# Kernel tuning notes

Measured on AMD Instinct MI355X. Metric: run time of the kernel, lower is better.

The kernel has to match this reference:

```python
import jax, jax.numpy as jnp
import numpy as np

E = 2048      # enc_size
B = 64        # number of output buffer slices (leaves)
STEPS = 2 * B - 1  # 63 reduces then 64 shifts


def _res(x, W, b):
    # ResLayer: residual + ReLU MLP, x: (E,)
    return x + jax.nn.relu(x @ W + b)


def setup_inputs() -> dict:
    key = jax.random.key(0)
    ks = jax.random.split(key, 12)
    s = 1.0 / np.sqrt(E)
    inp = {
        "input_encoding": jax.random.normal(ks[0], (E,), dtype=jnp.float32),
        # 63 ones (reduce) followed by 64 zeros (shift): valid shift-reduce tree
        "fixed_actions": jnp.concatenate([jnp.ones((B - 1,), jnp.int64 if jax.config.jax_enable_x64 else jnp.int32),
                                          jnp.zeros((B,), jnp.int64 if jax.config.jax_enable_x64 else jnp.int32)]),
        # act_scorer: ResLayer + Linear(E, 2)
        "act_res_W": jax.random.normal(ks[1], (E, E), jnp.float32) * s,
        "act_res_b": jnp.zeros((E,), jnp.float32),
        "act_W": jax.random.normal(ks[2], (E, 2), jnp.float32) * s,
        "act_b": jnp.zeros((2,), jnp.float32),
        # unreduce_l: two ResLayers
        "ul1_W": jax.random.normal(ks[3], (E, E), jnp.float32) * s,
        "ul1_b": jnp.zeros((E,), jnp.float32),
        "ul2_W": jax.random.normal(ks[4], (E, E), jnp.float32) * s,
        "ul2_b": jnp.zeros((E,), jnp.float32),
        # unreduce_r: two ResLayers
        "ur1_W": jax.random.normal(ks[5], (E, E), jnp.float32) * s,
        "ur1_b": jnp.zeros((E,), jnp.float32),
        "ur2_W": jax.random.normal(ks[6], (E, E), jnp.float32) * s,
        "ur2_b": jnp.zeros((E,), jnp.float32),
    }
    return inp


def reference(input_encoding, act_res_W, act_res_b, act_W, act_b,
              ul1_W, ul1_b, ul2_W, ul2_b, ur1_W, ur1_b, ur2_W, ur2_b,
              fixed_actions):
    # fixed_actions is a constant action sequence -> Python-level unroll of the
    # data-dependent stack machine (faithful to the torch while-loop).
    acts = np.asarray(fixed_actions)
    stack = [input_encoding]
    buffer_slices = []
    logit_rec = []
    for step in range(acts.shape[0]):
        a = int(acts[step])
        top = stack[-1]
        logits = _res(top, act_res_W, act_res_b) @ act_W + act_b  # (2,)
        score = jax.nn.softmax(logits)[a]
        st = 1.0 + score - jax.lax.stop_gradient(score)  # straight-through scale (fwd == 1)
        logit_rec.append(logits)
        if a == 0:  # shift: pop to buffer
            x = stack.pop()
            buffer_slices.append(x * st)
            if len(stack) == 0:
                break
        else:  # reduce: pop, push unreduce_r then unreduce_l
            prev = stack.pop()
            l = _res(_res(prev, ul1_W, ul1_b), ul2_W, ul2_b)
            r = _res(_res(prev, ur1_W, ur1_b), ur2_W, ur2_b)
            stack.append(r * st)
            stack.append(l * st)
    return jnp.stack(buffer_slices, 0), jnp.stack(logit_rec, 0)
```

## Files before the change

kernel.cpp:

```cpp
#include <hip/hip_runtime.h>

#define EN 2048
#define NCH 256
#define CTH 1024
#define SENT 0xFFFFFFFFu

#define T_OFF    0
#define H_OFF    (64 * EN)
#define FLG_OFF  (128 * EN)
#define HT_OFF   (129 * EN)
#define P_OFF    (256 * EN)

#define AL64(p)   __hip_atomic_load((const unsigned long long*)(p), __ATOMIC_RELAXED, __HIP_MEMORY_SCOPE_AGENT)
#define AL32(p)   __hip_atomic_load((const unsigned*)(p), __ATOMIC_RELAXED, __HIP_MEMORY_SCOPE_AGENT)
#define AS32(p,v) __hip_atomic_store((unsigned*)(p), (v), __ATOMIC_RELAXED, __HIP_MEMORY_SCOPE_AGENT)
#define AS64(p,v) __hip_atomic_store((unsigned long long*)(p), (v), __ATOMIC_RELAXED, __HIP_MEMORY_SCOPE_AGENT)

__device__ __forceinline__ float af(unsigned u) { return __uint_as_float(u); }

__device__ __forceinline__ void done_bar(unsigned* D, int b, int tid) {
    __syncthreads();
    if (tid < 64) {
        if (tid == 0) {
            asm volatile("s_waitcnt vmcnt(0)" ::: "memory");
            AS32(&D[b], 1u);
        }
        const unsigned long long* f = (const unsigned long long*)D;
        const unsigned long long GOOD = 0x0000000100000001ULL;
        for (long it = 0; it < 200000000L; ++it) {
            unsigned long long a = AL64(&f[tid * 2]);
            unsigned long long c = AL64(&f[tid * 2 + 1]);
            if (!__any((int)(a != GOOD || c != GOOD))) break;
        }
    }
    __syncthreads();
}

__device__ __forceinline__ void gemm64(
    const float* __restrict__ arow_thread, const float* __restrict__ Wmat,
    int k0base, int c0, float* __restrict__ Pslot, int nch, int tid,
    float (*As)[74], float (*Ws)[74])
{
    const int am   = tid >> 4;
    const int am_k = (tid & 15) * 2;
    const int wk   = tid >> 5;
    const int wq2  = (tid & 31) * 2;
    const int tr2  = tid >> 5, tc2 = tid & 31;
    float acc00 = 0.f, acc01 = 0.f, acc10 = 0.f, acc11 = 0.f;

    unsigned long long ra = AL64(arow_thread + k0base + am_k);
    float2 rw = *(const float2*)(Wmat + (size_t)(k0base + wk) * EN + c0 + wq2);

    for (int kt = 0; kt < nch; ++kt) {
        __syncthreads();
        As[am_k][am]     = af((unsigned)ra);
        As[am_k + 1][am] = af((unsigned)(ra >> 32));
        Ws[wk][wq2]      = rw.x;
        Ws[wk][wq2 + 1]  = rw.y;
        __syncthreads();
        if (kt + 1 < nch) {
            int k0 = k0base + (kt + 1) * 32;
            ra = AL64(arow_thread + k0 + am_k);
            rw = *(const float2*)(Wmat + (size_t)(k0 + wk) * EN + c0 + wq2);
        }
#pragma unroll
        for (int kk = 0; kk < 32; ++kk) {
            float2 a  = *(const float2*)&As[kk][tr2 * 2];
            float2 w2 = *(const float2*)&Ws[kk][tc2 * 2];
            acc00 += a.x * w2.x; acc01 += a.x * w2.y;
            acc10 += a.y * w2.x; acc11 += a.y * w2.y;
        }
    }
    unsigned long long p0 = ((unsigned long long)__float_as_uint(acc01) << 32) | __float_as_uint(acc00);
    unsigned long long p1 = ((unsigned long long)__float_as_uint(acc11) << 32) | __float_as_uint(acc10);
    AS64(Pslot + (size_t)(tr2 * 2) * EN + c0 + tc2 * 2, p0);
    AS64(Pslot + (size_t)(tr2 * 2 + 1) * EN + c0 + tc2 * 2, p1);
}

__global__ __launch_bounds__(CTH, 1) void mega_kernel(
    const float* __restrict__ x0,
    const float* __restrict__ ul1W, const float* __restrict__ ul1b,
    const float* __restrict__ ul2W, const float* __restrict__ ul2b,
    const float* __restrict__ ur1W, const float* __restrict__ ur1b,
    const float* __restrict__ ur2W, const float* __restrict__ ur2b,
    const float* __restrict__ arW,  const float* __restrict__ arb,
    const float* __restrict__ aW,   const float* __restrict__ ab,
    float* __restrict__ T, float* __restrict__ Hb, float* __restrict__ RT1,
    float* __restrict__ HT, float* __restrict__ P, unsigned* __restrict__ FLG,
    float* __restrict__ out)
{
    __shared__ __align__(16) float xs[EN];
    __shared__ __align__(16) float red_t[16][20];
    __shared__ float bias_s[16];
    __shared__ float As[32][74];
    __shared__ float Ws[32][74];
    __shared__ float lred[16][2];

    const int tid  = threadIdx.x;
    const int b    = blockIdx.x;
    const int lane = tid & 63;
    const int wv   = tid >> 6;

    {
        const int half  = b >> 7;
        const int idx   = b & 127;
        const int c0    = idx * 16;
        const int col   = tid & 15;
        const int chunk = tid >> 4;
        const float* Wg = half ? ul2W : ul1W;
        const float* bg = half ? ul2b : ul1b;

        float4 w[8];
#pragma unroll
        for (int j = 0; j < 8; ++j) {
            const float* wp = Wg + (size_t)(chunk * 32 + j * 4) * EN + c0 + col;
            w[j].x = wp[0]; w[j].y = wp[EN]; w[j].z = wp[2 * EN]; w[j].w = wp[3 * EN];
        }
        if (tid < 16) bias_s[tid] = bg[c0 + tid];

        for (int k = 1; k <= 63; ++k) {
            if (half == 0 && k == 1) {
                reinterpret_cast<float2*>(xs)[tid] = reinterpret_cast<const float2*>(x0)[tid];
            } else {
                const float* src = half ? (Hb + (size_t)k * EN) : (T + (size_t)(k - 1) * EN);
                const unsigned long long* s64 =
                    reinterpret_cast<const unsigned long long*>(src) + (size_t)wv * 64 + lane;
                unsigned long long v0 = AL64(s64), v1 = AL64(s64), vv;
                for (long it = 0;; ++it) {
                    { unsigned lo = (unsigned)v0, hi = (unsigned)(v0 >> 32);
                      if (!__any((int)(lo == SENT || hi == SENT))) { vv = v0; break; } }
                    v0 = AL64(s64);
                    { unsigned lo = (unsigned)v1, hi = (unsigned)(v1 >> 32);
                      if (!__any((int)(lo == SENT || hi == SENT))) { vv = v1; break; } }
                    v1 = AL64(s64);
                    if (it > 100000000L) { vv = v0; break; }
                }
                float2 xv;
                xv.x = af((unsigned)vv); xv.y = af((unsigned)(vv >> 32));
                reinterpret_cast<float2*>(xs)[tid] = xv;
            }
            __syncthreads();

            float s = 0.f;
            const float4* xv4 = reinterpret_cast<const float4*>(xs) + chunk * 8;
#pragma unroll
            for (int j = 0; j < 8; ++j) {
                float4 x4 = xv4[j];
                s += x4.x * w[j].x + x4.y * w[j].y + x4.z * w[j].z + x4.w * w[j].w;
            }
            s += __shfl_xor(s, 16, 64);
            s += __shfl_xor(s, 32, 64);
            if (lane < 16) red_t[lane][wv] = s;
            __syncthreads();

            if (wv == 0 && lane < 16) {
                float4 r0 = *(const float4*)&red_t[lane][0];
                float4 r1 = *(const float4*)&red_t[lane][4];
                float4 r2 = *(const float4*)&red_t[lane][8];
                float4 r3 = *(const float4*)&red_t[lane][12];
                float tot = ((r0.x + r0.y) + (r0.z + r0.w)) + ((r1.x + r1.y) + (r1.z + r1.w))
                          + ((r2.x + r2.y) + (r2.z + r2.w)) + ((r3.x + r3.y) + (r3.z + r3.w))
                          + bias_s[lane];
                float o = xs[c0 + lane] + fmaxf(tot, 0.f);
                float* dst = half ? (T + (size_t)k * EN) : (Hb + (size_t)k * EN);
                AS32(&dst[c0 + lane], __float_as_uint(o));
                if (half && k == 63) out[c0 + lane] = o;
                if (!half && k == 1) AS32(&T[c0 + lane], __float_as_uint(xs[c0 + lane]));
            }
        }
    }

    unsigned* D0 = FLG;            unsigned* D1 = FLG + 256;
    unsigned* D2 = FLG + 512;      unsigned* D3 = FLG + 768;
    unsigned* D4 = FLG + 1024;     unsigned* D5 = FLG + 1280;
    const int am = tid >> 4;

    {
        int ks = b >> 5, cc = b & 31;
        int ar = am > 62 ? 62 : am;
        gemm64(T + (size_t)ar * EN, ur1W, ks * 256, cc * 64, P + (size_t)ks * 64 * EN, 8, tid, As, Ws);
    }
    done_bar(D0, b, tid);

    if (tid < 504) {
        int m = tid >> 3, c = 8 * b + (tid & 7);
        float p = 0.f;
#pragma unroll
        for (int ks = 0; ks < 8; ++ks) p += af(AL32(P + ((size_t)ks * 64 + m) * EN + c));
        float tv = af(AL32(T + (size_t)m * EN + c));
        AS32(RT1 + (size_t)m * EN + c, __float_as_uint(tv + fmaxf(p + ur1b[c], 0.f)));
    }
    done_bar(D1, b, tid);

    {
        int ks = b >> 5, cc = b & 31;
        int ar = am > 62 ? 62 : am;
        gemm64(RT1 + (size_t)ar * EN, ur2W, ks * 256, cc * 64, P + (size_t)ks * 64 * EN, 8, tid, As, Ws);
    }
    done_bar(D2, b, tid);

    if (tid < 504) {
        int m = tid >> 3, c = 8 * b + (tid & 7);
        float p = 0.f;
#pragma unroll
        for (int ks = 0; ks < 8; ++ks) p += af(AL32(P + ((size_t)ks * 64 + m) * EN + c));
        float rv = af(AL32(RT1 + (size_t)m * EN + c));
        AS32(out + (size_t)(63 - m) * EN + c, __float_as_uint(rv + fmaxf(p + ur2b[c], 0.f)));
    }
    done_bar(D3, b, tid);

    {
        int ks = b >> 6, mh = (b >> 5) & 1, cc = b & 31;
        int rp = mh * 64 + am; if (rp > 126) rp = 126;
        const float* arow = (rp <= 63) ? (T + (size_t)rp * EN) : (out + (size_t)(rp - 63) * EN);
        gemm64(arow, arW, ks * 512, cc * 64, P + (size_t)(ks * 2 + mh) * 64 * EN, 16, tid, As, Ws);
    }
    done_bar(D4, b, tid);

    if (tid < 1016) {
        int m = tid >> 3, c = 8 * b + (tid & 7);
        int mh = m >> 6, mr = m & 63;
        float p = 0.f;
#pragma unroll
        for (int ks = 0; ks < 4; ++ks) p += af(AL32(P + ((size_t)(ks * 2 + mh) * 64 + mr) * EN + c));
        float tv = (m <= 63) ? af(AL32(T + (size_t)m * EN + c))
                             : af(AL32(out + (size_t)(m - 63) * EN + c));
        AS32(HT + (size_t)m * EN + c, __float_as_uint(tv + fmaxf(p + arb[c], 0.f)));
    }
    done_bar(D5, b, tid);

    if (b < 127) {
        const float* h = HT + (size_t)b * EN;
        unsigned long long hv = AL64(h + tid * 2);
        float h0 = af((unsigned)hv), h1 = af((unsigned)(hv >> 32));
        float4 w4 = *(const float4*)(aW + (size_t)tid * 4);
        float a0 = h0 * w4.x + h1 * w4.z;
        float a1 = h0 * w4.y + h1 * w4.w;
#pragma unroll
        for (int off = 32; off; off >>= 1) { a0 += __shfl_down(a0, off, 64); a1 += __shfl_down(a1, off, 64); }
        if (lane == 0) { lred[wv][0] = a0; lred[wv][1] = a1; }
        __syncthreads();
        if (tid == 0) {
            float s0 = ab[0], s1 = ab[1];
#pragma unroll
            for (int q = 0; q < 16; ++q) { s0 += lred[q][0]; s1 += lred[q][1]; }
            out[64 * EN + b * 2]     = s0;
            out[64 * EN + b * 2 + 1] = s1;
        }
    }
}

extern "C" void kernel_launch(void* const* d_in, const int* in_sizes, int n_in,
                              void* d_out, int out_size, void* d_ws, size_t ws_size,
                              hipStream_t stream)
{
    const float* x0   = (const float*)d_in[0];
    const float* arW  = (const float*)d_in[2];
    const float* arb  = (const float*)d_in[3];
    const float* aW   = (const float*)d_in[4];
    const float* ab   = (const float*)d_in[5];
    const float* ul1W = (const float*)d_in[6];
    const float* ul1b = (const float*)d_in[7];
    const float* ul2W = (const float*)d_in[8];
    const float* ul2b = (const float*)d_in[9];
    const float* ur1W = (const float*)d_in[10];
    const float* ur1b = (const float*)d_in[11];
    const float* ur2W = (const float*)d_in[12];
    const float* ur2b = (const float*)d_in[13];

    float* ws  = (float*)d_ws;
    float* out = (float*)d_out;
    float* T   = ws + T_OFF;
    float* Hb  = ws + H_OFF;
    float* RT1 = ws + H_OFF;
    float* HT  = ws + HT_OFF;
    float* P   = ws + P_OFF;
    unsigned* FLG = (unsigned*)(ws + FLG_OFF);

    hipMemsetAsync(ws, 0xFF, (size_t)(129 * EN) * sizeof(float), stream);

    void* args[] = { (void*)&x0, (void*)&ul1W, (void*)&ul1b, (void*)&ul2W, (void*)&ul2b,
                     (void*)&ur1W, (void*)&ur1b, (void*)&ur2W, (void*)&ur2b,
                     (void*)&arW, (void*)&arb, (void*)&aW, (void*)&ab,
                     (void*)&T, (void*)&Hb, (void*)&RT1, (void*)&HT, (void*)&P,
                     (void*)&FLG, (void*)&out };
    hipError_t err = hipLaunchCooperativeKernel(reinterpret_cast<void*>(mega_kernel),
                                                dim3(NCH), dim3(CTH), args, 0, stream);
    if (err != hipSuccess) {
        (void)hipGetLastError();
        mega_kernel<<<dim3(NCH), dim3(CTH), 0, stream>>>(
            x0, ul1W, ul1b, ul2W, ul2b, ur1W, ur1b, ur2W, ur2b,
            arW, arb, aW, ab, T, Hb, RT1, HT, P, FLG, out);
    }
}
```

Baseline: 394.4 us.

## Split batched GEMM phases into four K-quarters with 4x4 register tiles

Replaces the 2x2-per-thread GEMM helper with a templated version. It splits the 1024 threads into four K-quarter groups, each computing a 64x64 tile with 4x4 register blocking and wider vector loads. The partial sums are then reduced through shared memory before the packed atomic stores. This raises arithmetic intensity per shared-memory load in the batched ur1/ur2/act_res phases. In exchange it uses more LDS and adds an intra-block reduction step. The sentinel polling loop is also simplified to a single load per iteration with no timeout bailout, and some variables are renamed.

Measured after the change: 359.0 us. 9.0% less time.

```diff
diff --git a/kernel.cpp b/kernel.cpp
--- a/kernel.cpp
+++ b/kernel.cpp
@@ -17,6 +17,9 @@
 #define AS64(p,v) __hip_atomic_store((unsigned long long*)(p), (v), __ATOMIC_RELAXED, __HIP_MEMORY_SCOPE_AGENT)
 
 __device__ __forceinline__ float af(unsigned u) { return __uint_as_float(u); }
+__device__ __forceinline__ unsigned long long pk(float a, float b) {
+    return ((unsigned long long)__float_as_uint(b) << 32) | __float_as_uint(a);
+}
 
 __device__ __forceinline__ void done_bar(unsigned* D, int b, int tid) {
     __syncthreads();
@@ -36,45 +39,91 @@
     __syncthreads();
 }
 
-__device__ __forceinline__ void gemm64(
-    const float* __restrict__ arow_thread, const float* __restrict__ Wmat,
-    int k0base, int c0, float* __restrict__ Pslot, int nch, int tid,
-    float (*As)[74], float (*Ws)[74])
+template<int NKT>
+__device__ __forceinline__ void gemm_phase(
+    const float* __restrict__ a_stage_row,
+    const float* __restrict__ W, int kbase, int c0,
+    float* __restrict__ Pslot, int tid, float* __restrict__ GB)
 {
-    const int am   = tid >> 4;
-    const int am_k = (tid & 15) * 2;
-    const int wk   = tid >> 5;
-    const int wq2  = (tid & 31) * 2;
-    const int tr2  = tid >> 5, tc2 = tid & 31;
-    float acc00 = 0.f, acc01 = 0.f, acc10 = 0.f, acc11 = 0.f;
-
-    unsigned long long ra = AL64(arow_thread + k0base + am_k);
-    float2 rw = *(const float2*)(Wmat + (size_t)(k0base + wk) * EN + c0 + wq2);
-
-    for (int kt = 0; kt < nch; ++kt) {
+    const int kq  = tid >> 8;
+    const int rem = tid & 255;
+    const int ar  = rem >> 2;
+    const int ak8 = (rem & 3) * 8;
+    const int wk  = rem >> 3;
+    const int wc  = (rem & 7) * 8;
+    const int tr  = rem >> 4;
+    const int tc  = rem & 15;
+    float* As = GB + kq * (2 * 32 * 68);
+    float* Wt = As + 32 * 68;
+
+    float4 a0 = {0,0,0,0}, a1 = {0,0,0,0}, a2 = {0,0,0,0}, a3 = {0,0,0,0};
+
+    unsigned long long ra0, ra1, ra2, ra3;
+    float4 rw0, rw1;
+    {
+        ra0 = AL64(a_stage_row + kbase + ak8);
+        ra1 = AL64(a_stage_row + kbase + ak8 + 2);
+        ra2 = AL64(a_stage_row + kbase + ak8 + 4);
+        ra3 = AL64(a_stage_row + kbase + ak8 + 6);
+        const float* wp = W + (size_t)(kbase + wk) * EN + c0 + wc;
+        rw0 = *(const float4*)wp; rw1 = *(const float4*)(wp + 4);
+    }
+    for (int kt = 0; kt < NKT; ++kt) {
         __syncthreads();
-        As[am_k][am]     = af((unsigned)ra);
-        As[am_k + 1][am] = af((unsigned)(ra >> 32));
-        Ws[wk][wq2]      = rw.x;
-        Ws[wk][wq2 + 1]  = rw.y;
+        As[(ak8+0)*68+ar] = af((unsigned)ra0); As[(ak8+1)*68+ar] = af((unsigned)(ra0>>32));
+        As[(ak8+2)*68+ar] = af((unsigned)ra1); As[(ak8+3)*68+ar] = af((unsigned)(ra1>>32));
+        As[(ak8+4)*68+ar] = af((unsigned)ra2); As[(ak8+5)*68+ar] = af((unsigned)(ra2>>32));
+        As[(ak8+6)*68+ar] = af((unsigned)ra3); As[(ak8+7)*68+ar] = af((unsigned)(ra3>>32));
+        *(float4*)&Wt[wk*68+wc]     = rw0;
+        *(float4*)&Wt[wk*68+wc+4]  = rw1;
         __syncthreads();
-        if (kt + 1 < nch) {
-            int k0 = k0base + (kt + 1) * 32;
-            ra = AL64(arow_thread + k0 + am_k);
-            rw = *(const float2*)(Wmat + (size_t)(k0 + wk) * EN + c0 + wq2);
+        if (kt + 1 < NKT) {
+            int kb = kbase + (kt + 1) * 32;
+            ra0 = AL64(a_stage_row + kb + ak8);
+            ra1 = AL64(a_stage_row + kb + ak8 + 2);
+            ra2 = AL64(a_stage_row + kb + ak8 + 4);
+            ra3 = AL64(a_stage_row + kb + ak8 + 6);
+            const float* wp = W + (size_t)(kb + wk) * EN + c0 + wc;
+            rw0 = *(const float4*)wp; rw1 = *(const float4*)(wp + 4);
         }
 #pragma unroll
         for (int kk = 0; kk < 32; ++kk) {
-            float2 a  = *(const float2*)&As[kk][tr2 * 2];
-            float2 w2 = *(const float2*)&Ws[kk][tc2 * 2];
-            acc00 += a.x * w2.x; acc01 += a.x * w2.y;
-            acc10 += a.y * w2.x; acc11 += a.y * w2.y;
-        }
-    }
-    unsigned long long p0 = ((unsigned long long)__float_as_uint(acc01) << 32) | __float_as_uint(acc00);
-    unsigned long long p1 = ((unsigned long long)__float_as_uint(acc11) << 32) | __float_as_uint(acc10);
-    AS64(Pslot + (size_t)(tr2 * 2) * EN + c0 + tc2 * 2, p0);
-    AS64(Pslot + (size_t)(tr2 * 2 + 1) * EN + c0 + tc2 * 2, p1);
+            float4 av = *(const float4*)&As[kk*68 + tr*4];
+            float4 wv = *(const float4*)&Wt[kk*68 + tc*4];
+            a0.x += av.x*wv.x; a0.y += av.x*wv.y; a0.z += av.x*wv.z; a0.w += av.x*wv.w;
+            a1.x += av.y*wv.x; a1.y += av.y*wv.y; a1.z += av.y*wv.z; a1.w += av.y*wv.w;
+            a2.x += av.z*wv.x; a2.y += av.z*wv.y; a2.z += av.z*wv.z; a2.w += av.z*wv.w;
+            a3.x += av.w*wv.x; a3.y += av.w*wv.y; a3.z += av.w*wv.z; a3.w += av.w*wv.w;
+        }
+    }
+    __syncthreads();
+    if (kq > 0) {
+        float* d = GB + (kq - 1) * 4096 + rem;
+        d[0*256]=a0.x; d[1*256]=a0.y; d[2*256]=a0.z;  d[3*256]=a0.w;
+        d[4*256]=a1.x; d[5*256]=a1.y; d[6*256]=a1.z;  d[7*256]=a1.w;
+        d[8*256]=a2.x; d[9*256]=a2.y; d[10*256]=a2.z; d[11*256]=a2.w;
+        d[12*256]=a3.x; d[13*256]=a3.y; d[14*256]=a3.z; d[15*256]=a3.w;
+    }
+    __syncthreads();
+    if (kq == 0) {
+#pragma unroll
+        for (int q = 0; q < 3; ++q) {
+            const float* s = GB + q * 4096 + rem;
+            a0.x+=s[0*256]; a0.y+=s[1*256]; a0.z+=s[2*256];  a0.w+=s[3*256];
+            a1.x+=s[4*256]; a1.y+=s[5*256]; a1.z+=s[6*256];  a1.w+=s[7*256];
+            a2.x+=s[8*256]; a2.y+=s[9*256]; a2.z+=s[10*256]; a2.w+=s[11*256];
+            a3.x+=s[12*256]; a3.y+=s[13*256]; a3.z+=s[14*256]; a3.w+=s[15*256];
+        }
+        float* p0 = Pslot + (size_t)(tr*4    ) * EN + c0 + tc*4;
+        float* p1 = Pslot + (size_t)(tr*4 + 1) * EN + c0 + tc*4;
+        float* p2 = Pslot + (size_t)(tr*4 + 2) * EN + c0 + tc*4;
+        float* p3 = Pslot + (size_t)(tr*4 + 3) * EN + c0 + tc*4;
+        AS64(p0, pk(a0.x, a0.y)); AS64(p0 + 2, pk(a0.z, a0.w));
+        AS64(p1, pk(a1.x, a1.y)); AS64(p1 + 2, pk(a1.z, a1.w));
+        AS64(p2, pk(a2.x, a2.y)); AS64(p2 + 2, pk(a2.z, a2.w));
+        AS64(p3, pk(a3.x, a3.y)); AS64(p3 + 2, pk(a3.z, a3.w));
+    }
+    __syncthreads();
 }
 
 __global__ __launch_bounds__(CTH, 1) void mega_kernel(
@@ -92,8 +141,7 @@
     __shared__ __align__(16) float xs[EN];
     __shared__ __align__(16) float red_t[16][20];
     __shared__ float bias_s[16];
-    __shared__ float As[32][74];
-    __shared__ float Ws[32][74];
+    __shared__ __align__(16) float GB[4 * 2 * 32 * 68];
     __shared__ float lred[16][2];
 
     const int tid  = threadIdx.x;
@@ -125,18 +173,14 @@
                 const float* src = half ? (Hb + (size_t)k * EN) : (T + (size_t)(k - 1) * EN);
                 const unsigned long long* s64 =
                     reinterpret_cast<const unsigned long long*>(src) + (size_t)wv * 64 + lane;
-                unsigned long long v0 = AL64(s64), v1 = AL64(s64), vv;
-                for (long it = 0;; ++it) {
-                    { unsigned lo = (unsigned)v0, hi = (unsigned)(v0 >> 32);
-                      if (!__any((int)(lo == SENT || hi == SENT))) { vv = v0; break; } }
-                    v0 = AL64(s64);
-                    { unsigned lo = (unsigned)v1, hi = (unsigned)(v1 >> 32);
-                      if (!__any((int)(lo == SENT || hi == SENT))) { vv = v1; break; } }
-                    v1 = AL64(s64);
-                    if (it > 100000000L) { vv = v0; break; }
+                unsigned long long v;
+                for (;;) {
+                    v = AL64(s64);
+                    unsigned lo = (unsigned)v, hi = (unsigned)(v >> 32);
+                    if (!__any((int)(lo == SENT || hi == SENT))) break;
                 }
                 float2 xv;
-                xv.x = af((unsigned)vv); xv.y = af((unsigned)(vv >> 32));
+                xv.x = af((unsigned)v); xv.y = af((unsigned)(v >> 32));
                 reinterpret_cast<float2*>(xs)[tid] = xv;
             }
             __syncthreads();
@@ -173,12 +217,13 @@
     unsigned* D0 = FLG;            unsigned* D1 = FLG + 256;
     unsigned* D2 = FLG + 512;      unsigned* D3 = FLG + 768;
     unsigned* D4 = FLG + 1024;     unsigned* D5 = FLG + 1280;
-    const int am = tid >> 4;
-
-    {
-        int ks = b >> 5, cc = b & 31;
-        int ar = am > 62 ? 62 : am;
-        gemm64(T + (size_t)ar * EN, ur1W, ks * 256, cc * 64, P + (size_t)ks * 64 * EN, 8, tid, As, Ws);
+
+    {
+        const int rem = tid & 255, kq = tid >> 8;
+        int ar = rem >> 2; if (ar > 62) ar = 62;
+        int cc = b & 31, ks = b >> 5;
+        gemm_phase<2>(T + (size_t)ar * EN, ur1W, ks * 256 + kq * 64, cc * 64,
+                      P + (size_t)ks * 64 * EN, tid, GB);
     }
     done_bar(D0, b, tid);
 
@@ -193,9 +238,11 @@
     done_bar(D1, b, tid);
 
     {
-        int ks = b >> 5, cc = b & 31;
-        int ar = am > 62 ? 62 : am;
-        gemm64(RT1 + (size_t)ar * EN, ur2W, ks * 256, cc * 64, P + (size_t)ks * 64 * EN, 8, tid, As, Ws);
+        const int rem = tid & 255, kq = tid >> 8;
+        int ar = rem >> 2; if (ar > 62) ar = 62;
+        int cc = b & 31, ks = b >> 5;
+        gemm_phase<2>(RT1 + (size_t)ar * EN, ur2W, ks * 256 + kq * 64, cc * 64,
+                      P + (size_t)ks * 64 * EN, tid, GB);
     }
     done_bar(D2, b, tid);
 
@@ -210,10 +257,12 @@
     done_bar(D3, b, tid);
 
     {
-        int ks = b >> 6, mh = (b >> 5) & 1, cc = b & 31;
-        int rp = mh * 64 + am; if (rp > 126) rp = 126;
+        const int rem = tid & 255, kq = tid >> 8;
+        int cc = b & 31, mh = (b >> 5) & 1, ks = b >> 6;
+        int rp = mh * 64 + (rem >> 2); if (rp > 126) rp = 126;
         const float* arow = (rp <= 63) ? (T + (size_t)rp * EN) : (out + (size_t)(rp - 63) * EN);
-        gemm64(arow, arW, ks * 512, cc * 64, P + (size_t)(ks * 2 + mh) * 64 * EN, 16, tid, As, Ws);
+        gemm_phase<4>(arow, arW, ks * 512 + kq * 128, cc * 64,
+                      P + (size_t)(ks * 2 + mh) * 64 * EN, tid, GB);
     }
     done_bar(D4, b, tid);
 
@@ -234,18 +283,18 @@
         unsigned long long hv = AL64(h + tid * 2);
         float h0 = af((unsigned)hv), h1 = af((unsigned)(hv >> 32));
         float4 w4 = *(const float4*)(aW + (size_t)tid * 4);
-        float a0 = h0 * w4.x + h1 * w4.z;
-        float a1 = h0 * w4.y + h1 * w4.w;
-#pragma unroll
-        for (int off = 32; off; off >>= 1) { a0 += __shfl_down(a0, off, 64); a1 += __shfl_down(a1, off, 64); }
-        if (lane == 0) { lred[wv][0] = a0; lred[wv][1] = a1; }
+        float s0 = h0 * w4.x + h1 * w4.z;
+        float s1 = h0 * w4.y + h1 * w4.w;
+#pragma unroll
+        for (int off = 32; off; off >>= 1) { s0 += __shfl_down(s0, off, 64); s1 += __shfl_down(s1, off, 64); }
+        if (lane == 0) { lred[wv][0] = s0; lred[wv][1] = s1; }
         __syncthreads();
         if (tid == 0) {
-            float s0 = ab[0], s1 = ab[1];
-#pragma unroll
-            for (int q = 0; q < 16; ++q) { s0 += lred[q][0]; s1 += lred[q][1]; }
-            out[64 * EN + b * 2]     = s0;
-            out[64 * EN + b * 2 + 1] = s1;
+            float t0 = ab[0], t1 = ab[1];
+#pragma unroll
+            for (int q = 0; q < 16; ++q) { t0 += lred[q][0]; t1 += lred[q][1]; }
+            out[64 * EN + b * 2]     = t0;
+            out[64 * EN + b * 2 + 1] = t1;
         }
     }
 }
```
